# Optimization experiments

Measured on AMD Instinct MI355X. Metric: run time of the kernel, lower is better.

## Reference

```python
import jax, jax.numpy as jnp
import numpy as np

IN_DIM, H1, H2, N_CLASSES = 128, 100, 128, 19
BATCH, SEQ = 512, 256


def _lstm_relu(x, W, U, b, units):
    """Keras LSTM with activation='relu', recurrent_activation='sigmoid'.
    x: [B, T, D]. Returns (all hidden states [B, T, units], last hidden [B, units]).
    Gate order (Keras): i, f, g(cell candidate), o.
    """
    B = x.shape[0]
    h0 = jnp.zeros((B, units), x.dtype)
    c0 = jnp.zeros((B, units), x.dtype)

    # precompute input projections for all timesteps: [T, B, 4*units]
    zx = jnp.einsum('btd,dk->tbk', x, W) + b

    def step(carry, zx_t):
        h, c = carry
        z = zx_t + h @ U
        i, f, g, o = jnp.split(z, 4, axis=-1)
        i = jax.nn.sigmoid(i)
        f = jax.nn.sigmoid(f)
        g = jax.nn.relu(g)          # activation='relu'
        o = jax.nn.sigmoid(o)
        c = f * c + i * g
        h = o * jax.nn.relu(c)      # output activation is also relu
        return (h, c), h

    (h_last, _), hs = jax.lax.scan(step, (h0, c0), zx)
    return jnp.transpose(hs, (1, 0, 2)), h_last


def setup_inputs() -> dict:
    key = jax.random.key(0)
    ks = jax.random.split(key, 9)
    def w(k, shape, fan_in):
        return jax.random.normal(k, shape, jnp.float32) / np.sqrt(fan_in)
    x = jax.random.normal(ks[0], (BATCH, SEQ, IN_DIM), jnp.float32)
    return {
        'x': x,
        'W1': w(ks[1], (IN_DIM, 4 * H1), IN_DIM),
        'U1': w(ks[2], (H1, 4 * H1), H1),
        'b1': jnp.zeros((4 * H1,), jnp.float32),
        'W2': w(ks[3], (H1, 4 * H2), H1),
        'U2': w(ks[4], (H2, 4 * H2), H2),
        'b2': jnp.zeros((4 * H2,), jnp.float32),
        'Wd': w(ks[5], (H2, N_CLASSES), H2),
        'bd': jnp.zeros((N_CLASSES,), jnp.float32),
    }


def reference(x, W1, U1, b1, W2, U2, b2, Wd, bd):
    h1_seq, _ = _lstm_relu(x, W1, U1, b1, H1)      # [B, T, 100]
    _, h2 = _lstm_relu(h1_seq, W2, U2, b2, H2)     # [B, 128] (last step only)
    logits = h2 @ Wd + bd
    return jax.nn.softmax(logits, axis=-1)         # [B, 19]
```

## Files before the change

### kernel.cpp

```cpp
#include <hip/hip_runtime.h>
#include <math.h>


#define T_SEQ 256
#define BATCH 512
#define IN_DIM 128
#define H1 100
#define H2 128
#define NCLS 19

typedef float f4v __attribute__((ext_vector_type(4)));

__device__ __forceinline__ float sigmoidf_(float x) {
    return 1.0f / (1.0f + __expf(-x));
}
__device__ __forceinline__ float hsum4_(f4v v) {
    return (v.x + v.y) + (v.z + v.w);
}

#define REP4(M)  M(0) M(1) M(2) M(3)
#define REP7(M)  M(0) M(1) M(2) M(3) M(4) M(5) M(6)
#define REP8(M)  M(0) M(1) M(2) M(3) M(4) M(5) M(6) M(7)

template<int K, int N, bool SWAP>
__global__ __launch_bounds__(256, 4)
void proj_kernel(const float* __restrict__ A, const float* __restrict__ W,
                 const float* __restrict__ bias, float* __restrict__ out)
{
    constexpr int LDA = 132;
    constexpr int WCG = 260;
    __shared__ __align__(16) float As[32 * LDA];
    __shared__ __align__(16) float Ws[16 * WCG];
    const int tid = threadIdx.x;
    const int r0 = blockIdx.x * 128;
    const int c0 = blockIdx.y * 128;
    const int ty = tid >> 4, tx = tid & 15;

#define PACC(i) f4v accL##i = {0.f,0.f,0.f,0.f}; f4v accR##i = {0.f,0.f,0.f,0.f};
    REP8(PACC)
#undef PACC

    for (int kk = 0; kk < K; kk += 32) {
        __syncthreads();
#pragma unroll
        for (int i = 0; i < 4; ++i) {
            int idx = tid + i * 256;
            int row = idx >> 3, kg = idx & 7;
            int k = kk + kg * 4;
            f4v v = {0.f, 0.f, 0.f, 0.f};
            if (k < K) v = *(const f4v*)&A[(size_t)(r0 + row) * K + k];
            As[(kg * 4 + 0) * LDA + row] = v.x;
            As[(kg * 4 + 1) * LDA + row] = v.y;
            As[(kg * 4 + 2) * LDA + row] = v.z;
            As[(kg * 4 + 3) * LDA + row] = v.w;
        }
#pragma unroll
        for (int i = 0; i < 4; ++i) {
            int idx = tid + i * 256;
            int k = idx >> 5, q = idx & 31;
            int gk = kk + k, gc = c0 + q * 4;
            f4v v = {0.f, 0.f, 0.f, 0.f};
            if (gk < K && gc < N) v = *(const f4v*)&W[(size_t)gk * N + gc];
            int cg = q >> 1, half = q & 1;
            *(f4v*)&Ws[cg * WCG + k * 8 + half * 4] = v;
        }
        __syncthreads();
#pragma unroll
        for (int k = 0; k < 32; ++k) {
            f4v av0 = *(const f4v*)&As[k * LDA + ty * 8];
            f4v av1 = *(const f4v*)&As[k * LDA + ty * 8 + 4];
            f4v b0v = *(const f4v*)&Ws[tx * WCG + k * 8];
            f4v b1v = *(const f4v*)&Ws[tx * WCG + k * 8 + 4];
#define PFMA(i, s) accL##i += (s) * b0v; accR##i += (s) * b1v;
            PFMA(0, av0.x) PFMA(1, av0.y) PFMA(2, av0.z) PFMA(3, av0.w)
            PFMA(4, av1.x) PFMA(5, av1.y) PFMA(6, av1.z) PFMA(7, av1.w)
#undef PFMA
        }
    }

    const int cb = c0 + tx * 8;
    float b0 = (cb + 0 < N) ? bias[cb + 0] : 0.f;
    float b1 = (cb + 1 < N) ? bias[cb + 1] : 0.f;
    float b2 = (cb + 2 < N) ? bias[cb + 2] : 0.f;
    float b3 = (cb + 3 < N) ? bias[cb + 3] : 0.f;
    float b4 = (cb + 4 < N) ? bias[cb + 4] : 0.f;
    float b5 = (cb + 5 < N) ? bias[cb + 5] : 0.f;
    float b6 = (cb + 6 < N) ? bias[cb + 6] : 0.f;
    float b7 = (cb + 7 < N) ? bias[cb + 7] : 0.f;
    f4v bL = {b0, b1, b2, b3};
    f4v bR = {b4, b5, b6, b7};
#define PST(i) { \
        int r = r0 + ty * 8 + i; \
        size_t orow = SWAP ? ((size_t)(r & 255) * BATCH + (r >> 8)) : (size_t)r; \
        if (cb < N)     { f4v v = accL##i + bL; *(f4v*)&out[orow * N + cb] = v; } \
        if (cb + 4 < N) { f4v v = accR##i + bR; *(f4v*)&out[orow * N + cb + 4] = v; } }
    REP8(PST)
#undef PST
}

__device__ __forceinline__ f4v ldw_(const float* __restrict__ U1, int kb, int col) {
    int k0 = (kb + 0 < H1) ? kb + 0 : H1 - 1;
    int k1 = (kb + 1 < H1) ? kb + 1 : H1 - 1;
    int k2 = (kb + 2 < H1) ? kb + 2 : H1 - 1;
    int k3 = (kb + 3 < H1) ? kb + 3 : H1 - 1;
    f4v v;
    v.x = U1[(size_t)k0 * 400 + col];
    v.y = U1[(size_t)k1 * 400 + col];
    v.z = U1[(size_t)k2 * 400 + col];
    v.w = U1[(size_t)k3 * 400 + col];
    return v;
}

__global__ __launch_bounds__(512)
__attribute__((amdgpu_waves_per_eu(2, 2)))
void rec1_kernel(const float* __restrict__ zx,
                 const float* __restrict__ U1,
                 float* __restrict__ h1seq)
{
    const int row = blockIdx.x;
    const int tid = threadIdx.x;
    const int cl = tid >> 2;
    const int kq = tid & 3;
    const int cc = (cl < H1) ? cl : 0;
    __shared__ __align__(16) float hsP[2][112];

#define R1W(j) \
    f4v w0_##j = ldw_(U1, kq * 28 + 4 * (j), cc); \
    f4v w1_##j = ldw_(U1, kq * 28 + 4 * (j), 100 + cc); \
    f4v w2_##j = ldw_(U1, kq * 28 + 4 * (j), 200 + cc); \
    f4v w3_##j = ldw_(U1, kq * 28 + 4 * (j), 300 + cc);
    REP7(R1W)
#undef R1W
#define R1P(j) asm volatile("" : "+v"(w0_##j), "+v"(w1_##j), "+v"(w2_##j), "+v"(w3_##j));
    REP7(R1P)
#undef R1P

    if (tid < 112) { hsP[0][tid] = 0.0f; hsP[1][tid] = 0.0f; }
    const bool tail = (kq == 0) && (cl < H1);
    float cst = 0.0f;
    float zc0 = 0.f, zc1 = 0.f, zc2 = 0.f, zc3 = 0.f;
    if (tail) {
        const float* pz = zx + (size_t)row * 400 + cl;
        zc0 = pz[0]; zc1 = pz[100]; zc2 = pz[200]; zc3 = pz[300];
    }
    __syncthreads();

    for (int t = 0; t < T_SEQ; ++t) {
        float zn0 = 0.f, zn1 = 0.f, zn2 = 0.f, zn3 = 0.f;
        if (tail) {
            int tn = (t + 1 < T_SEQ) ? t + 1 : t;
            const float* pz = zx + ((size_t)tn * BATCH + row) * 400 + cl;
            zn0 = pz[0]; zn1 = pz[100]; zn2 = pz[200]; zn3 = pz[300];
        }

        const float* hb = hsP[t & 1];
        f4v s0 = {0.f, 0.f, 0.f, 0.f};
        f4v s1 = {0.f, 0.f, 0.f, 0.f};
        f4v s2 = {0.f, 0.f, 0.f, 0.f};
        f4v s3 = {0.f, 0.f, 0.f, 0.f};
#define R1F(j) { f4v hv = *(const f4v*)&hb[kq * 28 + 4 * (j)]; \
        s0 += hv * w0_##j; s1 += hv * w1_##j; s2 += hv * w2_##j; s3 += hv * w3_##j; }
        REP7(R1F)
#undef R1F
        float a0 = hsum4_(s0);
        float a1 = hsum4_(s1);
        float a2 = hsum4_(s2);
        float a3 = hsum4_(s3);
        a0 += __shfl_xor(a0, 1, 64); a0 += __shfl_xor(a0, 2, 64);
        a1 += __shfl_xor(a1, 1, 64); a1 += __shfl_xor(a1, 2, 64);
        a2 += __shfl_xor(a2, 1, 64); a2 += __shfl_xor(a2, 2, 64);
        a3 += __shfl_xor(a3, 1, 64); a3 += __shfl_xor(a3, 2, 64);

        if (tail) {
            float z0 = zc0 + a0;
            float z1 = zc1 + a1;
            float z2 = zc2 + a2;
            float z3 = zc3 + a3;
            float iv = sigmoidf_(z0);
            float fv = sigmoidf_(z1);
            float gv = fmaxf(z2, 0.0f);
            float ov = sigmoidf_(z3);
            cst = fv * cst + iv * gv;
            float h = ov * fmaxf(cst, 0.0f);
            hsP[(t + 1) & 1][cl] = h;
            h1seq[((size_t)t * BATCH + row) * H1 + cl] = h;
            zc0 = zn0; zc1 = zn1; zc2 = zn2; zc3 = zn3;
        }
        __syncthreads();
    }
}

template<bool INIT, bool LAST>
__global__ __launch_bounds__(512)
__attribute__((amdgpu_waves_per_eu(2, 2)))
void rec2_chunk(const float* __restrict__ zx,
                const float* __restrict__ U2,
                float* __restrict__ cbuf,
                float* __restrict__ hbuf,
                float* __restrict__ h2out,
                int tlen)
{
    const int row = blockIdx.x;
    const int tid = threadIdx.x;
    const int kq = tid >> 7;
    const int cl = tid & 127;
    __shared__ __align__(16) float hs[H2];
    __shared__ float zp[4 * 512];

#define R2_LD(j) \
    f4v w0_##j, w1_##j, w2_##j, w3_##j; { \
        const float* p = U2 + (size_t)(kq * 32 + 4 * j) * 512 + cl; \
        w0_##j = (f4v){p[0],   p[512],       p[1024],       p[1536]}; \
        w1_##j = (f4v){p[128], p[512 + 128], p[1024 + 128], p[1536 + 128]}; \
        w2_##j = (f4v){p[256], p[512 + 256], p[1024 + 256], p[1536 + 256]}; \
        w3_##j = (f4v){p[384], p[512 + 384], p[1024 + 384], p[1536 + 384]}; }
    REP8(R2_LD)
#undef R2_LD
#define R2P(j) asm volatile("" : "+v"(w0_##j), "+v"(w1_##j), "+v"(w2_##j), "+v"(w3_##j));
    REP8(R2P)
#undef R2P

    const bool upd = (tid < H2);
    float cst = 0.0f;
    if (upd) {
        if (INIT) {
            hs[tid] = 0.0f;
        } else {
            hs[tid] = hbuf[(size_t)row * H2 + tid];
            cst = cbuf[(size_t)row * H2 + tid];
        }
    }
    float zc0 = 0.f, zc1 = 0.f, zc2 = 0.f, zc3 = 0.f;
    if (upd) {
        const float* pz = zx + (size_t)row * 512 + tid;
        zc0 = pz[0]; zc1 = pz[128]; zc2 = pz[256]; zc3 = pz[384];
    }
    __syncthreads();

    for (int t = 0; t < tlen; ++t) {
        float zn0 = 0.f, zn1 = 0.f, zn2 = 0.f, zn3 = 0.f;
        if (upd) {
            int tn = (t + 1 < tlen) ? t + 1 : t;
            const float* pz = zx + ((size_t)tn * BATCH + row) * 512 + tid;
            zn0 = pz[0]; zn1 = pz[128]; zn2 = pz[256]; zn3 = pz[384];
        }

        f4v s0 = {0.f, 0.f, 0.f, 0.f};
        f4v s1 = {0.f, 0.f, 0.f, 0.f};
        f4v s2 = {0.f, 0.f, 0.f, 0.f};
        f4v s3 = {0.f, 0.f, 0.f, 0.f};
#define R2_FMA(j) { f4v hv = *(const f4v*)&hs[kq * 32 + 4 * j]; \
        s0 += hv * w0_##j; s1 += hv * w1_##j; s2 += hv * w2_##j; s3 += hv * w3_##j; }
        REP8(R2_FMA)
#undef R2_FMA
        zp[kq * 512 + cl]       = hsum4_(s0);
        zp[kq * 512 + cl + 128] = hsum4_(s1);
        zp[kq * 512 + cl + 256] = hsum4_(s2);
        zp[kq * 512 + cl + 384] = hsum4_(s3);
        __syncthreads();

        if (upd) {
            float z0 = zc0 + (zp[tid]        + zp[512 + tid])
                           + (zp[1024 + tid] + zp[1536 + tid]);
            float z1 = zc1 + (zp[tid + 128]  + zp[512 + tid + 128])
                           + (zp[1024 + tid + 128] + zp[1536 + tid + 128]);
            float z2 = zc2 + (zp[tid + 256]  + zp[512 + tid + 256])
                           + (zp[1024 + tid + 256] + zp[1536 + tid + 256]);
            float z3 = zc3 + (zp[tid + 384]  + zp[512 + tid + 384])
                           + (zp[1024 + tid + 384] + zp[1536 + tid + 384]);
            float iv = sigmoidf_(z0);
            float fv = sigmoidf_(z1);
            float gv = fmaxf(z2, 0.0f);
            float ov = sigmoidf_(z3);
            cst = fv * cst + iv * gv;
            hs[tid] = ov * fmaxf(cst, 0.0f);
            zc0 = zn0; zc1 = zn1; zc2 = zn2; zc3 = zn3;
        }
        __syncthreads();
    }

    if (upd) {
        float h = hs[tid];
        cbuf[(size_t)row * H2 + tid] = cst;
        hbuf[(size_t)row * H2 + tid] = h;
        if (LAST) h2out[(size_t)row * H2 + tid] = h;
    }
}

__global__ __launch_bounds__(64, 1)
void dense_softmax_kernel(const float* __restrict__ h2, const float* __restrict__ Wd,
                          const float* __restrict__ bd, float* __restrict__ out)
{
    const int b = blockIdx.x;
    const int k = threadIdx.x;
    __shared__ __align__(16) float hsm[H2];
    if (k < H2 / 4) ((f4v*)hsm)[k] = ((const f4v*)(h2 + (size_t)b * H2))[k];
    __syncthreads();

    float logit = -1e30f;
    if (k < NCLS) {
        float acc = bd[k];
#pragma unroll
        for (int d = 0; d < H2; ++d) acc += hsm[d] * Wd[d * NCLS + k];
        logit = acc;
    }
    float m = logit;
#pragma unroll
    for (int off = 32; off >= 1; off >>= 1) m = fmaxf(m, __shfl_xor(m, off, 64));
    float e = (k < NCLS) ? __expf(logit - m) : 0.0f;
    float s = e;
#pragma unroll
    for (int off = 32; off >= 1; off >>= 1) s += __shfl_xor(s, off, 64);
    if (k < NCLS) out[(size_t)b * NCLS + k] = e / s;
}

__global__ __launch_bounds__(448, 1)
void lstm1_fb(const float* __restrict__ x, const float* __restrict__ W1,
              const float* __restrict__ U1, const float* __restrict__ b1,
              float* __restrict__ h1out)
{
    const int b = blockIdx.x;
    const int k = threadIdx.x;
    __shared__ __align__(16) float xs[IN_DIM];
    __shared__ __align__(16) float hs[H1];
    __shared__ __align__(16) float zs[4 * H1];
    float w1r[IN_DIM];
    float u1r[H1];
    float bias = 0.0f;
    if (k < 4 * H1) {
        bias = b1[k];
#pragma unroll
        for (int d = 0; d < IN_DIM; ++d) w1r[d] = W1[d * (4 * H1) + k];
#pragma unroll
        for (int j = 0; j < H1; ++j) u1r[j] = U1[j * (4 * H1) + k];
    }
    if (k < H1) hs[k] = 0.0f;
    if (k < IN_DIM / 4)
        ((float4*)xs)[k] = ((const float4*)(x + ((size_t)b * T_SEQ) * IN_DIM))[k];
    float c = 0.0f;
    __syncthreads();
    for (int t = 0; t < T_SEQ; ++t) {
        if (k < 4 * H1) {
            float acc0 = bias, acc1 = 0.f, acc2 = 0.f, acc3 = 0.f;
#pragma unroll
            for (int q = 0; q < IN_DIM / 4; ++q) {
                float4 xv = ((const float4*)xs)[q];
                acc0 += xv.x * w1r[4 * q]; acc1 += xv.y * w1r[4 * q + 1];
                acc2 += xv.z * w1r[4 * q + 2]; acc3 += xv.w * w1r[4 * q + 3];
            }
#pragma unroll
            for (int q = 0; q < H1 / 4; ++q) {
                float4 hv = ((const float4*)hs)[q];
                acc0 += hv.x * u1r[4 * q]; acc1 += hv.y * u1r[4 * q + 1];
                acc2 += hv.z * u1r[4 * q + 2]; acc3 += hv.w * u1r[4 * q + 3];
            }
            float zv = (acc0 + acc1) + (acc2 + acc3);
            zs[k] = (k >= 2 * H1 && k < 3 * H1) ? fmaxf(zv, 0.0f) : sigmoidf_(zv);
        }
        __syncthreads();
        if (k < H1) {
            float i = zs[k], f = zs[k + H1], g = zs[k + 2 * H1], o = zs[k + 3 * H1];
            c = f * c + i * g;
            float h = o * fmaxf(c, 0.0f);
            hs[k] = h;
            h1out[((size_t)t * BATCH + b) * H1 + k] = h;
        }
        int tn = t + 1;
        if (tn < T_SEQ && k < IN_DIM / 4)
            ((float4*)xs)[k] = ((const float4*)(x + ((size_t)b * T_SEQ + tn) * IN_DIM))[k];
        __syncthreads();
    }
}

__global__ __launch_bounds__(512, 1)
void lstm2_fb(const float* __restrict__ h1in, const float* __restrict__ W2,
              const float* __restrict__ U2, const float* __restrict__ b2,
              float* __restrict__ h2out)
{
    const int b = blockIdx.x;
    const int k = threadIdx.x;
    __shared__ __align__(16) float ps[H1];
    __shared__ __align__(16) float hs[H2];
    __shared__ __align__(16) float zs[4 * H2];
    float w2r[H1];
    float u2r[H2];
    float bias = b2[k];
#pragma unroll
    for (int j = 0; j < H1; ++j) w2r[j] = W2[j * (4 * H2) + k];
#pragma unroll
    for (int j = 0; j < H2; ++j) u2r[j] = U2[j * (4 * H2) + k];
    if (k < H2) hs[k] = 0.0f;
    if (k < H1 / 4)
        ((float4*)ps)[k] = ((const float4*)(h1in + (size_t)b * H1))[k];
    float c = 0.0f;
    float hlast = 0.0f;
    __syncthreads();
    for (int t = 0; t < T_SEQ; ++t) {
        float acc0 = bias, acc1 = 0.f, acc2 = 0.f, acc3 = 0.f;
#pragma unroll
        for (int q = 0; q < H1 / 4; ++q) {
            float4 pv = ((const float4*)ps)[q];
            acc0 += pv.x * w2r[4 * q]; acc1 += pv.y * w2r[4 * q + 1];
            acc2 += pv.z * w2r[4 * q + 2]; acc3 += pv.w * w2r[4 * q + 3];
        }
#pragma unroll
        for (int q = 0; q < H2 / 4; ++q) {
            float4 hv = ((const float4*)hs)[q];
            acc0 += hv.x * u2r[4 * q]; acc1 += hv.y * u2r[4 * q + 1];
            acc2 += hv.z * u2r[4 * q + 2]; acc3 += hv.w * u2r[4 * q + 3];
        }
        float zv = (acc0 + acc1) + (acc2 + acc3);
        zs[k] = (k >= 2 * H2 && k < 3 * H2) ? fmaxf(zv, 0.0f) : sigmoidf_(zv);
        __syncthreads();
        if (k < H2) {
            float i = zs[k], f = zs[k + H2], g = zs[k + 2 * H2], o = zs[k + 3 * H2];
            c = f * c + i * g;
            hlast = o * fmaxf(c, 0.0f);
            hs[k] = hlast;
        }
        int tn = t + 1;
        if (tn < T_SEQ && k < H1 / 4)
            ((float4*)ps)[k] = ((const float4*)(h1in + ((size_t)tn * BATCH + b) * H1))[k];
        __syncthreads();
    }
    if (k < H2) h2out[(size_t)b * H2 + k] = hlast;
}

extern "C" void kernel_launch(void* const* d_in, const int* in_sizes, int n_in,
                              void* d_out, int out_size, void* d_ws, size_t ws_size,
                              hipStream_t stream) {
    const float* x  = (const float*)d_in[0];
    const float* W1 = (const float*)d_in[1];
    const float* U1 = (const float*)d_in[2];
    const float* b1 = (const float*)d_in[3];
    const float* W2 = (const float*)d_in[4];
    const float* U2 = (const float*)d_in[5];
    const float* b2 = (const float*)d_in[6];
    const float* Wd = (const float*)d_in[7];
    const float* bd = (const float*)d_in[8];
    float* out = (float*)d_out;

    const size_t zx_elems = (size_t)T_SEQ * BATCH * 400;
    const size_t h1_elems = (size_t)T_SEQ * BATCH * H1;
    const size_t st_elems = (size_t)BATCH * H2;
    const size_t need = (zx_elems + h1_elems + 3 * st_elems) * sizeof(float);

    if (ws_size >= need) {
        float* zxbuf = (float*)d_ws;
        float* h1buf = zxbuf + zx_elems;
        float* cbuf  = h1buf + h1_elems;
        float* hbuf  = cbuf + st_elems;
        float* h2buf = hbuf + st_elems;
        const int TC = T_SEQ / 2;

        hipLaunchKernelGGL((proj_kernel<IN_DIM, 4 * H1, true>), dim3(1024, 4), dim3(256), 0, stream,
                           x, W1, b1, zxbuf);
        hipLaunchKernelGGL(rec1_kernel, dim3(BATCH), dim3(512), 0, stream,
                           zxbuf, U1, h1buf);
        hipLaunchKernelGGL((proj_kernel<H1, 4 * H2, false>), dim3(512, 4), dim3(256), 0, stream,
                           h1buf, W2, b2, zxbuf);
        hipLaunchKernelGGL((rec2_chunk<true, false>), dim3(BATCH), dim3(512), 0, stream,
                           zxbuf, U2, cbuf, hbuf, h2buf, TC);
        hipLaunchKernelGGL((proj_kernel<H1, 4 * H2, false>), dim3(512, 4), dim3(256), 0, stream,
                           h1buf + (size_t)TC * BATCH * H1, W2, b2, zxbuf);
        hipLaunchKernelGGL((rec2_chunk<false, true>), dim3(BATCH), dim3(512), 0, stream,
                           zxbuf, U2, cbuf, hbuf, h2buf, TC);

        hipLaunchKernelGGL(dense_softmax_kernel, dim3(BATCH), dim3(64), 0, stream,
                           h2buf, Wd, bd, out);
    } else {
        float* h1buf = (float*)d_ws;
        float* h2buf = h1buf + h1_elems;
        hipLaunchKernelGGL(lstm1_fb, dim3(BATCH), dim3(448), 0, stream, x, W1, U1, b1, h1buf);
        hipLaunchKernelGGL(lstm2_fb, dim3(BATCH), dim3(512), 0, stream, h1buf, W2, U2, b2, h2buf);
        hipLaunchKernelGGL(dense_softmax_kernel, dim3(BATCH), dim3(64), 0, stream, h2buf, Wd, bd, out);
    }
}
```

Baseline: 1.271 ms.

## Split rec1 reduction across eight lanes per column and peel projection K tail

```diff
diff --git a/kernel.cpp b/kernel.cpp
--- a/kernel.cpp
+++ b/kernel.cpp
@@ -29,6 +29,8 @@
 {
     constexpr int LDA = 132;
     constexpr int WCG = 260;
+    constexpr int REM = K % 32;
+    constexpr int KFULL = K - REM;
     __shared__ __align__(16) float As[32 * LDA];
     __shared__ __align__(16) float Ws[16 * WCG];
     const int tid = threadIdx.x;
@@ -40,13 +42,57 @@
     REP8(PACC)
 #undef PACC
 
-    for (int kk = 0; kk < K; kk += 32) {
+#define PROJ_FMA_BODY \
+    { \
+        f4v b0v = *(const f4v*)&Ws[tx * WCG + k * 8]; \
+        f4v b1v = *(const f4v*)&Ws[tx * WCG + k * 8 + 4]; \
+        f4v av0 = *(const f4v*)&As[k * LDA + ty * 8]; \
+        f4v av1 = *(const f4v*)&As[k * LDA + ty * 8 + 4]; \
+        accL0 += av0.x * b0v; accR0 += av0.x * b1v; \
+        accL1 += av0.y * b0v; accR1 += av0.y * b1v; \
+        accL2 += av0.z * b0v; accR2 += av0.z * b1v; \
+        accL3 += av0.w * b0v; accR3 += av0.w * b1v; \
+        accL4 += av1.x * b0v; accR4 += av1.x * b1v; \
+        accL5 += av1.y * b0v; accR5 += av1.y * b1v; \
+        accL6 += av1.z * b0v; accR6 += av1.z * b1v; \
+        accL7 += av1.w * b0v; accR7 += av1.w * b1v; \
+    }
+
+    for (int kk = 0; kk < KFULL; kk += 32) {
         __syncthreads();
 #pragma unroll
         for (int i = 0; i < 4; ++i) {
             int idx = tid + i * 256;
             int row = idx >> 3, kg = idx & 7;
             int k = kk + kg * 4;
+            f4v v = *(const f4v*)&A[(size_t)(r0 + row) * K + k];
+            As[(kg * 4 + 0) * LDA + row] = v.x;
+            As[(kg * 4 + 1) * LDA + row] = v.y;
+            As[(kg * 4 + 2) * LDA + row] = v.z;
+            As[(kg * 4 + 3) * LDA + row] = v.w;
+        }
+#pragma unroll
+        for (int i = 0; i < 4; ++i) {
+            int idx = tid + i * 256;
+            int k = idx >> 5, q = idx & 31;
+            int gk = kk + k, gc = c0 + q * 4;
+            f4v v = {0.f, 0.f, 0.f, 0.f};
+            if (gc < N) v = *(const f4v*)&W[(size_t)gk * N + gc];
+            int cg = q >> 1, half = q & 1;
+            *(f4v*)&Ws[cg * WCG + k * 8 + half * 4] = v;
+        }
+        __syncthreads();
+#pragma unroll
+        for (int k = 0; k < 32; ++k) PROJ_FMA_BODY
+    }
+
+    if constexpr (REM > 0) {
+        __syncthreads();
+#pragma unroll
+        for (int i = 0; i < 4; ++i) {
+            int idx = tid + i * 256;
+            int row = idx >> 3, kg = idx & 7;
+            int k = KFULL + kg * 4;
             f4v v = {0.f, 0.f, 0.f, 0.f};
             if (k < K) v = *(const f4v*)&A[(size_t)(r0 + row) * K + k];
             As[(kg * 4 + 0) * LDA + row] = v.x;
@@ -58,7 +104,7 @@
         for (int i = 0; i < 4; ++i) {
             int idx = tid + i * 256;
             int k = idx >> 5, q = idx & 31;
-            int gk = kk + k, gc = c0 + q * 4;
+            int gk = KFULL + k, gc = c0 + q * 4;
             f4v v = {0.f, 0.f, 0.f, 0.f};
             if (gk < K && gc < N) v = *(const f4v*)&W[(size_t)gk * N + gc];
             int cg = q >> 1, half = q & 1;
@@ -66,17 +112,9 @@
         }
         __syncthreads();
 #pragma unroll
-        for (int k = 0; k < 32; ++k) {
-            f4v av0 = *(const f4v*)&As[k * LDA + ty * 8];
-            f4v av1 = *(const f4v*)&As[k * LDA + ty * 8 + 4];
-            f4v b0v = *(const f4v*)&Ws[tx * WCG + k * 8];
-            f4v b1v = *(const f4v*)&Ws[tx * WCG + k * 8 + 4];
-#define PFMA(i, s) accL##i += (s) * b0v; accR##i += (s) * b1v;
-            PFMA(0, av0.x) PFMA(1, av0.y) PFMA(2, av0.z) PFMA(3, av0.w)
-            PFMA(4, av1.x) PFMA(5, av1.y) PFMA(6, av1.z) PFMA(7, av1.w)
-#undef PFMA
-        }
-    }
+        for (int k = 0; k < REM; ++k) PROJ_FMA_BODY
+    }
+#undef PROJ_FMA_BODY
 
     const int cb = c0 + tx * 8;
     float b0 = (cb + 0 < N) ? bias[cb + 0] : 0.f;
@@ -111,31 +149,31 @@
     return v;
 }
 
-__global__ __launch_bounds__(512)
-__attribute__((amdgpu_waves_per_eu(2, 2)))
+__global__ __launch_bounds__(1024)
+__attribute__((amdgpu_waves_per_eu(4, 4)))
 void rec1_kernel(const float* __restrict__ zx,
                  const float* __restrict__ U1,
                  float* __restrict__ h1seq)
 {
     const int row = blockIdx.x;
     const int tid = threadIdx.x;
-    const int cl = tid >> 2;
-    const int kq = tid & 3;
+    const int cl = tid >> 3;
+    const int kq = tid & 7;
     const int cc = (cl < H1) ? cl : 0;
-    __shared__ __align__(16) float hsP[2][112];
+    __shared__ __align__(16) float hsP[2][8][20];
 
 #define R1W(j) \
-    f4v w0_##j = ldw_(U1, kq * 28 + 4 * (j), cc); \
-    f4v w1_##j = ldw_(U1, kq * 28 + 4 * (j), 100 + cc); \
-    f4v w2_##j = ldw_(U1, kq * 28 + 4 * (j), 200 + cc); \
-    f4v w3_##j = ldw_(U1, kq * 28 + 4 * (j), 300 + cc);
-    REP7(R1W)
+    f4v w0_##j = ldw_(U1, kq * 16 + 4 * (j), cc); \
+    f4v w1_##j = ldw_(U1, kq * 16 + 4 * (j), 100 + cc); \
+    f4v w2_##j = ldw_(U1, kq * 16 + 4 * (j), 200 + cc); \
+    f4v w3_##j = ldw_(U1, kq * 16 + 4 * (j), 300 + cc);
+    REP4(R1W)
 #undef R1W
 #define R1P(j) asm volatile("" : "+v"(w0_##j), "+v"(w1_##j), "+v"(w2_##j), "+v"(w3_##j));
-    REP7(R1P)
+    REP4(R1P)
 #undef R1P
 
-    if (tid < 112) { hsP[0][tid] = 0.0f; hsP[1][tid] = 0.0f; }
+    if (tid < 320) ((float*)hsP)[tid] = 0.0f;
     const bool tail = (kq == 0) && (cl < H1);
     float cst = 0.0f;
     float zc0 = 0.f, zc1 = 0.f, zc2 = 0.f, zc3 = 0.f;
@@ -153,36 +191,32 @@
             zn0 = pz[0]; zn1 = pz[100]; zn2 = pz[200]; zn3 = pz[300];
         }
 
-        const float* hb = hsP[t & 1];
+        const float* hb = &hsP[t & 1][0][0];
         f4v s0 = {0.f, 0.f, 0.f, 0.f};
         f4v s1 = {0.f, 0.f, 0.f, 0.f};
         f4v s2 = {0.f, 0.f, 0.f, 0.f};
         f4v s3 = {0.f, 0.f, 0.f, 0.f};
-#define R1F(j) { f4v hv = *(const f4v*)&hb[kq * 28 + 4 * (j)]; \
+#define R1F(j) { f4v hv = *(const f4v*)&hb[kq * 20 + 4 * (j)]; \
         s0 += hv * w0_##j; s1 += hv * w1_##j; s2 += hv * w2_##j; s3 += hv * w3_##j; }
-        REP7(R1F)
+        REP4(R1F)
 #undef R1F
         float a0 = hsum4_(s0);
         float a1 = hsum4_(s1);
         float a2 = hsum4_(s2);
         float a3 = hsum4_(s3);
-        a0 += __shfl_xor(a0, 1, 64); a0 += __shfl_xor(a0, 2, 64);
-        a1 += __shfl_xor(a1, 1, 64); a1 += __shfl_xor(a1, 2, 64);
-        a2 += __shfl_xor(a2, 1, 64); a2 += __shfl_xor(a2, 2, 64);
-        a3 += __shfl_xor(a3, 1, 64); a3 += __shfl_xor(a3, 2, 64);
+        a0 += __shfl_xor(a0, 1, 64); a0 += __shfl_xor(a0, 2, 64); a0 += __shfl_xor(a0, 4, 64);
+        a1 += __shfl_xor(a1, 1, 64); a1 += __shfl_xor(a1, 2, 64); a1 += __shfl_xor(a1, 4, 64);
+        a2 += __shfl_xor(a2, 1, 64); a2 += __shfl_xor(a2, 2, 64); a2 += __shfl_xor(a2, 4, 64);
+        a3 += __shfl_xor(a3, 1, 64); a3 += __shfl_xor(a3, 2, 64); a3 += __shfl_xor(a3, 4, 64);
 
         if (tail) {
-            float z0 = zc0 + a0;
-            float z1 = zc1 + a1;
-            float z2 = zc2 + a2;
-            float z3 = zc3 + a3;
-            float iv = sigmoidf_(z0);
-            float fv = sigmoidf_(z1);
-            float gv = fmaxf(z2, 0.0f);
-            float ov = sigmoidf_(z3);
+            float iv = sigmoidf_(zc0 + a0);
+            float fv = sigmoidf_(zc1 + a1);
+            float gv = fmaxf(zc2 + a2, 0.0f);
+            float ov = sigmoidf_(zc3 + a3);
             cst = fv * cst + iv * gv;
             float h = ov * fmaxf(cst, 0.0f);
-            hsP[(t + 1) & 1][cl] = h;
+            hsP[(t + 1) & 1][cl >> 4][cl & 15] = h;
             h1seq[((size_t)t * BATCH + row) * H1 + cl] = h;
             zc0 = zn0; zc1 = zn1; zc2 = zn2; zc3 = zn3;
         }
@@ -455,7 +489,7 @@
 
         hipLaunchKernelGGL((proj_kernel<IN_DIM, 4 * H1, true>), dim3(1024, 4), dim3(256), 0, stream,
                            x, W1, b1, zxbuf);
-        hipLaunchKernelGGL(rec1_kernel, dim3(BATCH), dim3(512), 0, stream,
+        hipLaunchKernelGGL(rec1_kernel, dim3(BATCH), dim3(1024), 0, stream,
                            zxbuf, U1, h1buf);
         hipLaunchKernelGGL((proj_kernel<H1, 4 * H2, false>), dim3(512, 4), dim3(256), 0, stream,
                            h1buf, W2, b2, zxbuf);
```

New measurement: 1.461 ms. 15.0% more time.
